# Performance work log

Measured on AMD Instinct MI355X. Metric: run time of the kernel, lower is better.

The kernel has to match this reference:

```python
import jax, jax.numpy as jnp
from jax import lax
import numpy as np

B, DIM, HEADS, H, W = 4, 384, 8, 128, 128


def conv2d(x, w, b, groups=1, pad=0):
    # x: NCHW, w: OIHW (I = in_channels // groups)
    y = lax.conv_general_dilated(
        x, w, window_strides=(1, 1), padding=[(pad, pad), (pad, pad)],
        dimension_numbers=("NCHW", "OIHW", "NCHW"), feature_group_count=groups)
    return y + b[None, :, None, None]


def _l2norm(x, eps=1e-12):
    # torch F.normalize(dim=-1): x / max(||x||_2, eps)
    n = jnp.sqrt(jnp.sum(x * x, axis=-1, keepdims=True))
    return x / jnp.maximum(n, eps)


def setup_inputs() -> dict:
    key = jax.random.key(0)
    ks = jax.random.split(key, 8)
    s = 0.02
    d = DIM
    return {
        "x": jax.random.normal(ks[0], (B, d, H, W), jnp.float32),
        "feature": jax.random.normal(ks[1], (B, d, H, W), jnp.float32),
        "qkv_w": jax.random.normal(ks[2], (3 * d, d, 1, 1), jnp.float32) * s,
        "qkv_b": jnp.zeros((3 * d,), jnp.float32),
        "dw_w": jax.random.normal(ks[3], (3 * d, 1, 3, 3), jnp.float32) * s,  # depthwise, groups=3d
        "dw_b": jnp.zeros((3 * d,), jnp.float32),
        "qdw_w": jax.random.normal(ks[4], (2 * d, 1, 3, 3), jnp.float32) * s,  # depthwise, groups=2d
        "qdw_b": jnp.zeros((2 * d,), jnp.float32),
        "qpw_w": jax.random.normal(ks[5], (d, 2 * d, 1, 1), jnp.float32) * s,
        "qpw_b": jnp.zeros((d,), jnp.float32),
        "proj_w": jax.random.normal(ks[6], (d, d, 1, 1), jnp.float32) * s,
        "proj_b": jnp.zeros((d,), jnp.float32),
        "temperature": jnp.ones((HEADS, 1, 1), jnp.float32),
        "K": 24,  # top-k count == int(C * 0.5) with C = DIM // HEADS = 48
    }


def reference(x, feature, qkv_w, qkv_b, dw_w, dw_b, qdw_w, qdw_b,
              qpw_w, qpw_b, proj_w, proj_b, temperature, K):
    b, c, h, w = x.shape
    # qkv = dwconv3x3(conv1x1(x))
    qkv = conv2d(conv2d(x, qkv_w, qkv_b), dw_w, dw_b, groups=3 * c, pad=1)
    q, k, v = jnp.split(qkv, 3, axis=1)
    # q branch: dwconv3x3 on cat([q, feature]) -> GELU(exact) -> 1x1 conv
    qf = conv2d(jnp.concatenate([q, feature], axis=1), qdw_w, qdw_b, groups=2 * c, pad=1)
    qf = jax.nn.gelu(qf, approximate=False)
    q = conv2d(qf, qpw_w, qpw_b)

    def heads(t):
        return t.reshape(b, HEADS, c // HEADS, h * w)  # b head C (h w)

    q = _l2norm(heads(q))
    k = _l2norm(heads(k))
    v = heads(v)
    # channel attention: [b,head,C,C]
    attn = jnp.einsum("bhcn,bhdn->bhcd", q, k) * temperature
    vals, idx = lax.top_k(attn, K)
    neg = jnp.full_like(attn, -jnp.inf)
    attn = jnp.put_along_axis(neg, idx, vals, axis=-1, inplace=False)
    attn = jax.nn.softmax(attn, axis=-1)
    out = jnp.einsum("bhcd,bhdn->bhcn", attn, v).reshape(b, c, h, w)
    return conv2d(out, proj_w, proj_b)
```

## Files before the change

kernel.cpp:

```cpp
#include <hip/hip_runtime.h>

using u16 = unsigned short;
typedef __attribute__((ext_vector_type(8))) __bf16 bf16x8;
typedef __attribute__((ext_vector_type(4))) float  f32x4;
typedef __attribute__((ext_vector_type(8))) u16    u16x8;
typedef __attribute__((ext_vector_type(4))) u16    u16x4;

#define NB   4
#define DIM  384
#define NPIX 16384

__device__ __forceinline__ u16 f2bf(float f) {
  return __builtin_bit_cast(u16, (__bf16)f);
}
__device__ __forceinline__ float bf2f(u16 u) {
  return (float)__builtin_bit_cast(__bf16, u);
}
__device__ __forceinline__ void gload16(const void* g, void* l) {
  __builtin_amdgcn_global_load_lds(
      (const __attribute__((address_space(1))) void*)g,
      (__attribute__((address_space(3))) void*)l, 16, 0, 0);
}

__global__ void k_cvt2(const float* __restrict__ s, u16* __restrict__ hi,
                       u16* __restrict__ lo, int n) {
  int i = blockIdx.x * 256 + threadIdx.x;
  if (i < n) {
    float v = s[i];
    u16 h = f2bf(v);
    hi[i] = h;
    lo[i] = f2bf(v - bf2f(h));
  }
}

__global__ void k_splitx(const float* __restrict__ x, u16* __restrict__ xhi,
                         u16* __restrict__ xlo) {
  __shared__ float tile[64][33];
  const int tid = threadIdx.x;
  const int n0 = blockIdx.x * 32, c0 = blockIdx.y * 64, b = blockIdx.z;
  const int tj = tid & 31, ti = tid >> 5;
  const float* xp = x + ((size_t)b * DIM + c0) * NPIX + n0;
  #pragma unroll
  for (int i = 0; i < 8; ++i) {
    const int c = i * 8 + ti;
    tile[c][tj] = xp[(size_t)c * NPIX + tj];
  }
  __syncthreads();
  const int px = tid >> 3, sl = tid & 7;
  u16x8 ph, pl;
  #pragma unroll
  for (int e = 0; e < 8; ++e) {
    const float v = tile[sl * 8 + e][px];
    const u16 h = f2bf(v);
    ph[e] = h;
    pl[e] = f2bf(v - bf2f(h));
  }
  const size_t off = ((size_t)b * NPIX + n0 + px) * DIM + c0 + sl * 8;
  *(u16x8*)(xhi + off) = ph;
  *(u16x8*)(xlo + off) = pl;
}

template<int OUTMODE>
__global__ __launch_bounds__(256, 4)
void k_gemmS(const u16* __restrict__ A, const u16* __restrict__ B,
             void* __restrict__ Out, const float* __restrict__ bias,
             int M, int N, int Kd, size_t Astride)
{
  __shared__ u16 lA[128 * 64];
  __shared__ u16 lB[128 * 64];
  const int tid = threadIdx.x, wid = tid >> 6, lane = tid & 63;
  const int GX = gridDim.x, GY = gridDim.y;
  const int W = GX * GY * (int)gridDim.z;
  const int w = blockIdx.x + GX * (blockIdx.y + GY * blockIdx.z);
  const int nw = (w & 7) * (W >> 3) + (w >> 3);
  const int mt = nw % GY;
  const int rest = nw / GY;
  const int ntile = rest % GX;
  const int b = rest / GX;
  const int m0 = mt * 128, n0 = ntile * 128;

  const int srow = lane >> 3;
  const int sslot = (lane & 7) ^ srow;
  const size_t rowA = (size_t)(m0 + wid * 32 + srow) * Kd + sslot * 8 +
                      (size_t)b * Astride;
  const size_t rowB = ((size_t)b * N + n0 + wid * 32 + srow) * Kd + sslot * 8;
  u16* lAw = &lA[(wid * 32) * 64];
  u16* lBw = &lB[(wid * 32) * 64];
  const int wm = (wid & 1) * 64, wn = (wid >> 1) * 64;
  const int cl = lane & 15, rl = lane >> 4;
  const int sxa = cl & 7;

  f32x4 acc[4][4];
  const f32x4 fz = {0.f, 0.f, 0.f, 0.f};
  #pragma unroll
  for (int i = 0; i < 4; ++i)
    #pragma unroll
    for (int j = 0; j < 4; ++j) acc[i][j] = fz;

  const int nk = Kd >> 6;
  for (int kt = 0; kt < nk; ++kt) {
    const u16* Ap = A + rowA + kt * 64;
    const u16* Bp = B + rowB + kt * 64;
    __syncthreads();
    #pragma unroll
    for (int i = 0; i < 4; ++i) {
      gload16(Ap + (size_t)(i * 8) * Kd, lAw + i * 8 * 64);
      gload16(Bp + (size_t)(i * 8) * Kd, lBw + i * 8 * 64);
    }
    __syncthreads();
    #pragma unroll
    for (int ks = 0; ks < 2; ++ks) {
      bf16x8 av[4], bv[4];
      #pragma unroll
      for (int i = 0; i < 4; ++i) {
        av[i] = *(const bf16x8*)&lA[(wm + i * 16 + cl) * 64 + ((ks * 4 + rl) ^ sxa) * 8];
        bv[i] = *(const bf16x8*)&lB[(wn + i * 16 + cl) * 64 + ((ks * 4 + rl) ^ sxa) * 8];
      }
      #pragma unroll
      for (int i = 0; i < 4; ++i)
        #pragma unroll
        for (int j = 0; j < 4; ++j)
          acc[i][j] = __builtin_amdgcn_mfma_f32_16x16x32_bf16(av[i], bv[j], acc[i][j], 0, 0, 0);
    }
  }

  #pragma unroll
  for (int i = 0; i < 4; ++i) {
    #pragma unroll
    for (int j = 0; j < 4; ++j) {
      #pragma unroll
      for (int r = 0; r < 4; ++r) {
        const int m = m0 + wm + i * 16 + rl * 4 + r;
        const int n = n0 + wn + j * 16 + cl;
        const float v = acc[i][j][r] + bias[m];
        const size_t o = ((size_t)b * M + m) * N + n;
        if (OUTMODE == 0) ((float*)Out)[o] = v;
        else ((u16*)Out)[o] = f2bf(v);
      }
    }
  }
}

template<int OUTMODE, bool SSQ>
__global__ __launch_bounds__(256, 4)
void k_gemmP(const u16* __restrict__ Ahi, const u16* __restrict__ Alo,
             const u16* __restrict__ Bhi, const u16* __restrict__ Blo,
             void* __restrict__ Out, u16* __restrict__ OutLo,
             const float* __restrict__ bias, float* __restrict__ ssq,
             int M, int N, int Kd)
{
  __shared__ u16 lA[128 * 64];
  __shared__ u16 lB[128 * 64];
  const int tid = threadIdx.x, wid = tid >> 6, lane = tid & 63;
  const int GX = gridDim.x, GY = gridDim.y;
  const int W = GX * GY * (int)gridDim.z;
  const int w = blockIdx.x + GX * (blockIdx.y + GY * blockIdx.z);
  const int nw = (w & 7) * (W >> 3) + (w >> 3);
  const int mt = nw % GY;
  const int rest = nw / GY;
  const int ntile = rest % GX;
  const int b = rest / GX;
  const int m0 = mt * 128, n0 = ntile * 128;

  const int srow = lane >> 3;
  const int sp = (lane & 7) ^ srow;
  const int scol = (sp & 3) * 8;
  const u16* baseA = (sp < 4) ? Ahi : Alo;
  const u16* baseB = (sp < 4) ? Bhi : Blo;
  const u16* srcA[4];
  const u16* srcB[4];
  #pragma unroll
  for (int i = 0; i < 4; ++i) {
    srcA[i] = baseA + (size_t)(m0 + wid * 32 + i * 8 + srow) * Kd + scol;
    srcB[i] = baseB + ((size_t)b * N + n0 + wid * 32 + i * 8 + srow) * Kd + scol;
  }
  u16* lAw = &lA[(wid * 32) * 64];
  u16* lBw = &lB[(wid * 32) * 64];
  const int wm = (wid & 1) * 64, wn = (wid >> 1) * 64;
  const int cl = lane & 15, rl = lane >> 4;
  const int ph = rl ^ (cl & 7);

  f32x4 acc[4][4];
  const f32x4 fz = {0.f, 0.f, 0.f, 0.f};
  #pragma unroll
  for (int i = 0; i < 4; ++i)
    #pragma unroll
    for (int j = 0; j < 4; ++j) acc[i][j] = fz;

  const int nk = Kd >> 5;
  for (int kt = 0; kt < nk; ++kt) {
    __syncthreads();
    #pragma unroll
    for (int i = 0; i < 4; ++i) {
      gload16(srcA[i] + kt * 32, lAw + i * 8 * 64);
      gload16(srcB[i] + kt * 32, lBw + i * 8 * 64);
    }
    __syncthreads();
    bf16x8 avh[4], bvh[4], avl[4], bvl[4];
    #pragma unroll
    for (int i = 0; i < 4; ++i) {
      avh[i] = *(const bf16x8*)&lA[(wm + i * 16 + cl) * 64 + ph * 8];
      bvh[i] = *(const bf16x8*)&lB[(wn + i * 16 + cl) * 64 + ph * 8];
    }
    #pragma unroll
    for (int i = 0; i < 4; ++i)
      #pragma unroll
      for (int j = 0; j < 4; ++j)
        acc[i][j] = __builtin_amdgcn_mfma_f32_16x16x32_bf16(avh[i], bvh[j], acc[i][j], 0, 0, 0);
    #pragma unroll
    for (int i = 0; i < 4; ++i)
      avl[i] = *(const bf16x8*)&lA[(wm + i * 16 + cl) * 64 + (ph ^ 4) * 8];
    #pragma unroll
    for (int i = 0; i < 4; ++i)
      #pragma unroll
      for (int j = 0; j < 4; ++j)
        acc[i][j] = __builtin_amdgcn_mfma_f32_16x16x32_bf16(avl[i], bvh[j], acc[i][j], 0, 0, 0);
    #pragma unroll
    for (int i = 0; i < 4; ++i)
      bvl[i] = *(const bf16x8*)&lB[(wn + i * 16 + cl) * 64 + (ph ^ 4) * 8];
    #pragma unroll
    for (int i = 0; i < 4; ++i)
      #pragma unroll
      for (int j = 0; j < 4; ++j)
        acc[i][j] = __builtin_amdgcn_mfma_f32_16x16x32_bf16(avh[i], bvl[j], acc[i][j], 0, 0, 0);
  }

  float sq[4][4];
  if (SSQ) {
    #pragma unroll
    for (int i = 0; i < 4; ++i)
      #pragma unroll
      for (int r = 0; r < 4; ++r) sq[i][r] = 0.f;
  }
  #pragma unroll
  for (int i = 0; i < 4; ++i) {
    #pragma unroll
    for (int j = 0; j < 4; ++j) {
      #pragma unroll
      for (int r = 0; r < 4; ++r) {
        const int m = m0 + wm + i * 16 + rl * 4 + r;
        const int n = n0 + wn + j * 16 + cl;
        const float v = acc[i][j][r] + bias[m];
        if (SSQ) sq[i][r] += v * v;
        const size_t o = ((size_t)b * M + m) * N + n;
        if (OUTMODE == 0) ((float*)Out)[o] = v;
        else {
          u16 h = f2bf(v);
          ((u16*)Out)[o] = h;
          OutLo[o] = f2bf(v - bf2f(h));
        }
      }
    }
  }
  if (SSQ) {
    #pragma unroll
    for (int i = 0; i < 4; ++i) {
      #pragma unroll
      for (int r = 0; r < 4; ++r) {
        float s = sq[i][r];
        s += __shfl_xor(s, 1);
        s += __shfl_xor(s, 2);
        s += __shfl_xor(s, 4);
        s += __shfl_xor(s, 8);
        if (cl == 0)
          atomicAdd(&ssq[(size_t)b * M + m0 + wm + i * 16 + rl * 4 + r], s);
      }
    }
  }
}

__device__ __forceinline__ void row_acc_f32(const float* __restrict__ rowp,
    int x0, float w0, float w1, float w2,
    float& o0, float& o1, float& o2, float& o3)
{
  float4 r = *(const float4*)(rowp + x0);
  float lm = __shfl_up(r.w, 1);   if (x0 == 0)   lm = 0.f;
  float rt = __shfl_down(r.x, 1); if (x0 == 124) rt = 0.f;
  o0 = fmaf(lm,  w0, fmaf(r.x, w1, fmaf(r.y, w2, o0)));
  o1 = fmaf(r.x, w0, fmaf(r.y, w1, fmaf(r.z, w2, o1)));
  o2 = fmaf(r.y, w0, fmaf(r.z, w1, fmaf(r.w, w2, o2)));
  o3 = fmaf(r.z, w0, fmaf(r.w, w1, fmaf(rt,  w2, o3)));
}
__device__ __forceinline__ void row_acc_bf16(const u16* __restrict__ rowp,
    int x0, float w0, float w1, float w2,
    float& o0, float& o1, float& o2, float& o3)
{
  u16x4 rv = *(const u16x4*)(rowp + x0);
  float r0 = bf2f(rv[0]), r1 = bf2f(rv[1]), r2 = bf2f(rv[2]), r3 = bf2f(rv[3]);
  float lm = __shfl_up(r3, 1);   if (x0 == 0)   lm = 0.f;
  float rt = __shfl_down(r0, 1); if (x0 == 124) rt = 0.f;
  o0 = fmaf(lm, w0, fmaf(r0, w1, fmaf(r1, w2, o0)));
  o1 = fmaf(r0, w0, fmaf(r1, w1, fmaf(r2, w2, o1)));
  o2 = fmaf(r1, w0, fmaf(r2, w1, fmaf(r3, w2, o2)));
  o3 = fmaf(r2, w0, fmaf(r3, w1, fmaf(rt, w2, o3)));
}

__global__ __launch_bounds__(256, 4)
void k_dw3qk(const float* __restrict__ src, const float* __restrict__ w9,
             const float* __restrict__ bias, float* __restrict__ qdwbuf,
             u16* __restrict__ khi, u16* __restrict__ klo,
             float* __restrict__ ssqk)
{
  const int tid = threadIdx.x, wv = tid >> 6, lane = tid & 63;
  const int whw = blockIdx.x + 16 * (blockIdx.y + 96 * blockIdx.z);
  const int g = (whw & 7) + 8 * (whw >> 7);
  const int xchunk = (whw >> 3) & 15;
  const int cg = g % 96, b = g / 96;
  const int n0 = xchunk * 1024 + tid * 4;
  const int h = n0 >> 7, x0 = n0 & 127;
  const int c0 = cg * 8;
  const int hm = (h > 0) ? h - 1 : 0, hp = (h < 127) ? h + 1 : 127;
  const float topf = (h > 0) ? 1.f : 0.f, botf = (h < 127) ? 1.f : 0.f;
  const float* base = src + ((size_t)b * 768 + c0) * NPIX;
  const bool isk = (c0 >= 384);
  float ssl[8];
  #pragma unroll
  for (int s = 0; s < 8; ++s) {
    const int c = c0 + s;
    const float* sp = base + (size_t)s * NPIX;
    const float* wc = w9 + c * 9;
    const float bz = bias[c];
    float o0 = bz, o1 = bz, o2 = bz, o3 = bz;
    row_acc_f32(sp + hm * 128, x0, wc[0] * topf, wc[1] * topf, wc[2] * topf, o0, o1, o2, o3);
    row_acc_f32(sp + h  * 128, x0, wc[3], wc[4], wc[5], o0, o1, o2, o3);
    row_acc_f32(sp + hp * 128, x0, wc[6] * botf, wc[7] * botf, wc[8] * botf, o0, o1, o2, o3);
    if (!isk) {
      float4 ov = make_float4(o0, o1, o2, o3);
      *(float4*)(qdwbuf + ((size_t)b * 384 + c) * NPIX + n0) = ov;
      ssl[s] = 0.f;
    } else {
      ssl[s] = o0 * o0 + o1 * o1 + o2 * o2 + o3 * o3;
      u16x4 ph, pl;
      float oo[4] = {o0, o1, o2, o3};
      #pragma unroll
      for (int j = 0; j < 4; ++j) {
        u16 hv = f2bf(oo[j]);
        ph[j] = hv;
        pl[j] = f2bf(oo[j] - bf2f(hv));
      }
      const size_t off = ((size_t)b * 384 + (c - 384)) * NPIX + n0;
      *(u16x4*)(khi + off) = ph;
      *(u16x4*)(klo + off) = pl;
    }
  }
  if (isk) {
    __shared__ float sred[4][8];
    #pragma unroll
    for (int s = 0; s < 8; ++s) {
      float v = ssl[s];
      #pragma unroll
      for (int off = 32; off; off >>= 1) v += __shfl_down(v, off);
      if (lane == 0) sred[wv][s] = v;
    }
    __syncthreads();
    if (tid < 8) {
      float t = sred[0][tid] + sred[1][tid] + sred[2][tid] + sred[3][tid];
      atomicAdd(&ssqk[(size_t)b * DIM + (c0 - 384) + tid], t);
    }
  }
}

__global__ __launch_bounds__(512, 4)
void k_dw3vT(const u16* __restrict__ src, const float* __restrict__ w9,
             const float* __restrict__ bias, u16* __restrict__ vT)
{
  __shared__ u16 th[256 * 64];
  const int tid = threadIdx.x, wv = tid >> 6, lane = tid & 63;
  const int whw = blockIdx.x + 64 * (blockIdx.y + 6 * blockIdx.z);
  const int g = (whw & 7) + 8 * (whw >> 9);
  const int xchunk = (whw >> 3) & 63;
  const int cg = g % 6, b = g / 6;
  const int npx0 = xchunk * 256;
  const int n0 = npx0 + lane * 4;
  const int h = n0 >> 7, x0 = n0 & 127;
  const int c0 = cg * 64 + wv * 8;
  const int hm = (h > 0) ? h - 1 : 0, hp = (h < 127) ? h + 1 : 127;
  const float topf = (h > 0) ? 1.f : 0.f, botf = (h < 127) ? 1.f : 0.f;
  const u16* base = src + ((size_t)b * 384 + c0) * NPIX;
  u16x8 vh[4];
  #pragma unroll
  for (int s = 0; s < 8; ++s) {
    const int c = c0 + s;
    const u16* sp = base + (size_t)s * NPIX;
    const float* wc = w9 + c * 9;
    const float bz = bias[c];
    float o0 = bz, o1 = bz, o2 = bz, o3 = bz;
    row_acc_bf16(sp + hm * 128, x0, wc[0] * topf, wc[1] * topf, wc[2] * topf, o0, o1, o2, o3);
    row_acc_bf16(sp + h  * 128, x0, wc[3], wc[4], wc[5], o0, o1, o2, o3);
    row_acc_bf16(sp + hp * 128, x0, wc[6] * botf, wc[7] * botf, wc[8] * botf, o0, o1, o2, o3);
    vh[0][s] = f2bf(o0); vh[1][s] = f2bf(o1);
    vh[2][s] = f2bf(o2); vh[3][s] = f2bf(o3);
  }
  const int sl = (wv ^ (lane & 7)) * 8;
  #pragma unroll
  for (int j = 0; j < 4; ++j) {
    const int px = lane * 4 + j;
    *(u16x8*)&th[px * 64 + sl] = vh[j];
  }
  __syncthreads();
  if (tid < 256) {
    const int px = tid;
    u16* dst = vT + ((size_t)b * NPIX + npx0 + px) * 384 + cg * 64;
    const int rsw = (px >> 2) & 7;
    #pragma unroll
    for (int s = 0; s < 8; ++s)
      *(u16x8*)(dst + s * 8) = *(const u16x8*)&th[px * 64 + ((s ^ rsw) * 8)];
  }
}

__global__ __launch_bounds__(512, 4)
void k_qdw2(const float* __restrict__ qdwbuf, const float* __restrict__ feat,
            const float* __restrict__ w9, const float* __restrict__ bias,
            u16* __restrict__ qfhi, u16* __restrict__ qflo)
{
  __shared__ u16 th[256 * 64];
  __shared__ u16 tl[256 * 64];
  const int tid = threadIdx.x, wv = tid >> 6, lane = tid & 63;
  const int whw = blockIdx.x + 64 * (blockIdx.y + 12 * blockIdx.z);
  const int g = (whw & 7) + 8 * (whw >> 9);
  const int xchunk = (whw >> 3) & 63;
  const int cg = g % 12, b = g / 12;
  const int npx0 = xchunk * 256;
  const int n0 = npx0 + lane * 4;
  const int h = n0 >> 7, x0 = n0 & 127;
  const int c0 = cg * 64 + wv * 8;
  const int hm = (h > 0) ? h - 1 : 0, hp = (h < 127) ? h + 1 : 127;
  const float topf = (h > 0) ? 1.f : 0.f, botf = (h < 127) ? 1.f : 0.f;
  const bool isq = (c0 < 384);
  const float* base = isq ? (qdwbuf + ((size_t)b * 384 + c0) * NPIX)
                          : (feat   + ((size_t)b * 384 + (c0 - 384)) * NPIX);
  u16x8 vh[4], vl[4];
  #pragma unroll
  for (int s = 0; s < 8; ++s) {
    const int c = c0 + s;
    const float* sp = base + (size_t)s * NPIX;
    const float* wc = w9 + c * 9;
    const float bz = bias[c];
    float o0 = bz, o1 = bz, o2 = bz, o3 = bz;
    row_acc_f32(sp + hm * 128, x0, wc[0] * topf, wc[1] * topf, wc[2] * topf, o0, o1, o2, o3);
    row_acc_f32(sp + h  * 128, x0, wc[3], wc[4], wc[5], o0, o1, o2, o3);
    row_acc_f32(sp + hp * 128, x0, wc[6] * botf, wc[7] * botf, wc[8] * botf, o0, o1, o2, o3);
    float oo[4] = {o0, o1, o2, o3};
    #pragma unroll
    for (int j = 0; j < 4; ++j) {
      const float a = oo[j];
      const float g2 = 0.5f * a * (1.0f + erff(a * 0.70710678118654752440f));
      const u16 hv = f2bf(g2);
      vh[j][s] = hv;
      vl[j][s] = f2bf(g2 - bf2f(hv));
    }
  }
  const int sl = (wv ^ (lane & 7)) * 8;
  #pragma unroll
  for (int j = 0; j < 4; ++j) {
    const int px = lane * 4 + j;
    *(u16x8*)&th[px * 64 + sl] = vh[j];
    *(u16x8*)&tl[px * 64 + sl] = vl[j];
  }
  __syncthreads();
  const int sel = tid >> 8;
  const int px = tid & 255;
  const u16* srcb = sel ? tl : th;
  u16* dst = (sel ? qflo : qfhi) +
             ((size_t)b * NPIX + npx0 + px) * 768 + cg * 64;
  const int rsw = (px >> 2) & 7;
  #pragma unroll
  for (int s = 0; s < 8; ++s)
    *(u16x8*)(dst + s * 8) = *(const u16x8*)&srcb[px * 64 + ((s ^ rsw) * 8)];
}

__global__ __launch_bounds__(256)
void k_qk3(const u16* __restrict__ qhi, const u16* __restrict__ qlo,
           const u16* __restrict__ khi, const u16* __restrict__ klo,
           float* __restrict__ part)
{
  const int wid = threadIdx.x >> 6, lane = threadIdx.x & 63;
  const int bh = blockIdx.y;
  const int b = bh >> 3, hd = bh & 7;
  const size_t base = ((size_t)b * 384 + hd * 48) * NPIX;
  const int cl = lane & 15, rl = lane >> 4;
  f32x4 acc[3][3];
  const f32x4 fz = {0.f, 0.f, 0.f, 0.f};
  #pragma unroll
  for (int i = 0; i < 3; ++i)
    #pragma unroll
    for (int j = 0; j < 3; ++j) acc[i][j] = fz;
  for (int ck = 0; ck < 2; ++ck) {
    const int n0 = (blockIdx.x * 2 + ck) * 512 + wid * 128;
    #pragma unroll
    for (int ks = 0; ks < 4; ++ks) {
      const int nn = n0 + ks * 32 + rl * 8;
      bf16x8 ah[3], al[3], bh16[3], bl16[3];
      #pragma unroll
      for (int i = 0; i < 3; ++i) {
        const size_t ro = base + (size_t)(i * 16 + cl) * NPIX + nn;
        ah[i]   = *(const bf16x8*)&qhi[ro];
        al[i]   = *(const bf16x8*)&qlo[ro];
        bh16[i] = *(const bf16x8*)&khi[ro];
        bl16[i] = *(const bf16x8*)&klo[ro];
      }
      #pragma unroll
      for (int i = 0; i < 3; ++i)
        #pragma unroll
        for (int j = 0; j < 3; ++j) {
          acc[i][j] = __builtin_amdgcn_mfma_f32_16x16x32_bf16(ah[i], bh16[j], acc[i][j], 0, 0, 0);
          acc[i][j] = __builtin_amdgcn_mfma_f32_16x16x32_bf16(ah[i], bl16[j], acc[i][j], 0, 0, 0);
          acc[i][j] = __builtin_amdgcn_mfma_f32_16x16x32_bf16(al[i], bh16[j], acc[i][j], 0, 0, 0);
        }
    }
  }
  float* pp = part + ((size_t)bh * 64 + blockIdx.x * 4 + wid) * 2304;
  #pragma unroll
  for (int i = 0; i < 3; ++i)
    #pragma unroll
    for (int j = 0; j < 3; ++j)
      #pragma unroll
      for (int r = 0; r < 4; ++r)
        pp[(i * 16 + rl * 4 + r) * 48 + (j * 16 + cl)] = acc[i][j][r];
}

__global__ void k_qkred(const float* __restrict__ part, float* __restrict__ raw)
{
  const int bh = blockIdx.x;
  const int p = blockIdx.y * 256 + threadIdx.x;
  const float* pp = part + (size_t)bh * 64 * 2304 + p;
  float s = 0.f;
  #pragma unroll 8
  for (int w = 0; w < 64; ++w) s += pp[(size_t)w * 2304];
  raw[(size_t)bh * 2304 + p] = s;
}

__global__ void k_attn2(const float* __restrict__ raw, const float* __restrict__ ssq_q,
                        const float* __restrict__ ssq_k, const float* __restrict__ temp,
                        const int* __restrict__ Kp, const float* __restrict__ W,
                        u16* __restrict__ WaHi)
{
  __shared__ float at[48 * 49];
  const int bh = blockIdx.x, b = bh >> 3, hd = bh & 7;
  const int tid = threadIdx.x, wv = tid >> 6, lane = tid & 63;
  const int K = *Kp;
  const int d = lane;
  const bool act = (d < 48);
  const float ki = act ? 1.0f / fmaxf(sqrtf(ssq_k[b * DIM + hd * 48 + d]), 1e-12f) : 0.f;
  const float tmp = temp[hd];
  for (int r = 0; r < 12; ++r) {
    const int c = wv * 12 + r;
    const float qi = tmp / fmaxf(sqrtf(ssq_q[b * DIM + hd * 48 + c]), 1e-12f);
    const float v = act ? raw[(size_t)bh * 2304 + c * 48 + d] * qi * ki : -3.0e38f;
    int rank = 0;
    #pragma unroll
    for (int e = 0; e < 48; ++e) {
      const float ve = __shfl(v, e);
      rank += (ve > v || (ve == v && e < d)) ? 1 : 0;
    }
    const bool keep = act && (rank < K);
    float mx = keep ? v : -3.0e38f;
    #pragma unroll
    for (int off = 32; off; off >>= 1) mx = fmaxf(mx, __shfl_xor(mx, off));
    const float ex = keep ? expf(v - mx) : 0.f;
    float sum = ex;
    #pragma unroll
    for (int off = 32; off; off >>= 1) sum += __shfl_xor(sum, off);
    const float rs = 1.0f / sum;
    if (act) at[c * 49 + d] = ex * rs;
  }
  __syncthreads();
  for (int idx = tid; idx < 384 * 48; idx += 256) {
    const int m = idx / 48, dd = idx - m * 48;
    const float* wr = W + (size_t)m * 384 + hd * 48;
    float s = 0.f;
    #pragma unroll
    for (int c = 0; c < 48; ++c) s += wr[c] * at[c * 49 + dd];
    WaHi[((size_t)b * 384 + m) * 384 + hd * 48 + dd] = f2bf(s);
  }
}

extern "C" void kernel_launch(void* const* d_in, const int* in_sizes, int n_in,
                              void* d_out, int out_size, void* d_ws, size_t ws_size,
                              hipStream_t stream)
{
  (void)in_sizes; (void)n_in; (void)out_size; (void)ws_size;
  const float* x      = (const float*)d_in[0];
  const float* feat   = (const float*)d_in[1];
  const float* qkv_w  = (const float*)d_in[2];
  const float* qkv_b  = (const float*)d_in[3];
  const float* dw_w   = (const float*)d_in[4];
  const float* dw_b   = (const float*)d_in[5];
  const float* qdw_w  = (const float*)d_in[6];
  const float* qdw_b  = (const float*)d_in[7];
  const float* qpw_w  = (const float*)d_in[8];
  const float* qpw_b  = (const float*)d_in[9];
  const float* proj_w = (const float*)d_in[10];
  const float* proj_b = (const float*)d_in[11];
  const float* temp   = (const float*)d_in[12];
  const int*   Kp     = (const int*)d_in[13];

  char* ws = (char*)d_ws;
  const size_t HALF = 50331648;

  u16* WqkvHi = (u16*)ws;
  u16* WqkvLo = WqkvHi + 1152 * 384;
  u16* WqpwHi = WqkvLo + 1152 * 384;
  u16* WqpwLo = WqpwHi + 384 * 768;
  float* ssqQ = (float*)(ws + 3244032);
  float* ssqK = ssqQ + NB * DIM;
  float* raw  = ssqK + NB * DIM;
  u16* WaHi   = (u16*)(ws + (4ull << 20));
  char* R1 = ws + (16ull << 20);
  u16* xThi = (u16*)R1;
  u16* xTlo = (u16*)(R1 + HALF);
  float* qdwbuf = (float*)R1;
  u16* qHi = (u16*)R1;
  u16* qLo = (u16*)(R1 + HALF);
  char* R2 = ws + (112ull << 20);
  float* qkpre = (float*)R2;
  u16* qfHi = (u16*)R2;
  u16* qfLo = (u16*)(R2 + 2 * HALF);
  float* part = (float*)R2;
  u16* vT   = (u16*)R2;
  u16* vpre = (u16*)(ws + (304ull << 20));
  u16* kHi = (u16*)d_out;
  u16* kLo = kHi + (size_t)NB * DIM * NPIX;

  hipMemsetAsync(ssqQ, 0, 2 * NB * DIM * sizeof(float), stream);
  k_cvt2<<<dim3(1728), 256, 0, stream>>>(qkv_w, WqkvHi, WqkvLo, 1152 * 384);
  k_cvt2<<<dim3(1152), 256, 0, stream>>>(qpw_w, WqpwHi, WqpwLo, 384 * 768);
  k_splitx<<<dim3(512, 6, NB), 256, 0, stream>>>(x, xThi, xTlo);
  k_gemmP<0, false><<<dim3(128, 6, NB), 256, 0, stream>>>(WqkvHi, WqkvLo, xThi, xTlo,
      (void*)qkpre, nullptr, qkv_b, nullptr, 768, NPIX, 384);
  k_gemmS<1><<<dim3(128, 3, NB), 256, 0, stream>>>(WqkvHi + (size_t)768 * 384,
      xThi, (void*)vpre, qkv_b + 768, 384, NPIX, 384, 0);
  k_dw3qk<<<dim3(16, 96, NB), 256, 0, stream>>>(qkpre, dw_w, dw_b, qdwbuf, kHi, kLo, ssqK);
  k_qdw2<<<dim3(64, 12, NB), 512, 0, stream>>>(qdwbuf, feat, qdw_w, qdw_b, qfHi, qfLo);
  k_gemmP<2, true><<<dim3(128, 3, NB), 256, 0, stream>>>(WqpwHi, WqpwLo, qfHi, qfLo,
      (void*)qHi, qLo, qpw_b, ssqQ, 384, NPIX, 768);
  k_qk3<<<dim3(16, 32), 256, 0, stream>>>(qHi, qLo, kHi, kLo, part);
  k_qkred<<<dim3(32, 9), 256, 0, stream>>>(part, raw);
  k_attn2<<<dim3(32), 256, 0, stream>>>(raw, ssqQ, ssqK, temp, Kp, proj_w, WaHi);
  k_dw3vT<<<dim3(64, 6, NB), 512, 0, stream>>>(vpre, dw_w + 768 * 9, dw_b + 768, vT);
  k_gemmS<0><<<dim3(128, 3, NB), 256, 0, stream>>>(WaHi, vT,
      d_out, proj_b, 384, NPIX, 384, (size_t)384 * 384);
}
```

Baseline: 813.4 us.

## Double-buffer LDS in split-bf16 GEMM with async prefetch two tiles ahead

Turns the k_gemmP main loop into a two-stage LDS pipeline. Global-to-LDS loads for tile kt+2 are issued right after tile kt's MFMAs, and explicit vmcnt waits plus raw barriers replace the paired __syncthreads, so memory latency overlaps compute. The doubled LDS footprint lowers the launch-bounds occupancy hint from 4 to 2 blocks per CU, which reduces latency hiding across blocks. The vmcnt(8) count relies on each thread issuing exactly 8 loads per stage.

```diff
diff --git a/kernel.cpp b/kernel.cpp
--- a/kernel.cpp
+++ b/kernel.cpp
@@ -142,15 +142,15 @@
 }
 
 template<int OUTMODE, bool SSQ>
-__global__ __launch_bounds__(256, 4)
+__global__ __launch_bounds__(256, 2)
 void k_gemmP(const u16* __restrict__ Ahi, const u16* __restrict__ Alo,
              const u16* __restrict__ Bhi, const u16* __restrict__ Blo,
              void* __restrict__ Out, u16* __restrict__ OutLo,
              const float* __restrict__ bias, float* __restrict__ ssq,
              int M, int N, int Kd)
 {
-  __shared__ u16 lA[128 * 64];
-  __shared__ u16 lB[128 * 64];
+  __shared__ u16 lA[2][128 * 64];
+  __shared__ u16 lB[2][128 * 64];
   const int tid = threadIdx.x, wid = tid >> 6, lane = tid & 63;
   const int GX = gridDim.x, GY = gridDim.y;
   const int W = GX * GY * (int)gridDim.z;
@@ -174,8 +174,7 @@
     srcA[i] = baseA + (size_t)(m0 + wid * 32 + i * 8 + srow) * Kd + scol;
     srcB[i] = baseB + ((size_t)b * N + n0 + wid * 32 + i * 8 + srow) * Kd + scol;
   }
-  u16* lAw = &lA[(wid * 32) * 64];
-  u16* lBw = &lB[(wid * 32) * 64];
+  const int woff = (wid * 32) * 64;
   const int wm = (wid & 1) * 64, wn = (wid >> 1) * 64;
   const int cl = lane & 15, rl = lane >> 4;
   const int ph = rl ^ (cl & 7);
@@ -188,19 +187,33 @@
     for (int j = 0; j < 4; ++j) acc[i][j] = fz;
 
   const int nk = Kd >> 5;
+
+  #pragma unroll
+  for (int i = 0; i < 4; ++i) {
+    gload16(srcA[i], &lA[0][woff + i * 8 * 64]);
+    gload16(srcB[i], &lB[0][woff + i * 8 * 64]);
+  }
+  #pragma unroll
+  for (int i = 0; i < 4; ++i) {
+    gload16(srcA[i] + 32, &lA[1][woff + i * 8 * 64]);
+    gload16(srcB[i] + 32, &lB[1][woff + i * 8 * 64]);
+  }
+
   for (int kt = 0; kt < nk; ++kt) {
-    __syncthreads();
+    if (kt + 1 < nk) {
+      asm volatile("s_waitcnt vmcnt(8)" ::: "memory");
+    } else {
+      asm volatile("s_waitcnt vmcnt(0)" ::: "memory");
+    }
+    __builtin_amdgcn_s_barrier();
+    __builtin_amdgcn_sched_barrier(0);
+    const u16* bA = lA[kt & 1];
+    const u16* bB = lB[kt & 1];
+    bf16x8 avh[4], bvh[4], avl[4], bvl[4];
     #pragma unroll
     for (int i = 0; i < 4; ++i) {
-      gload16(srcA[i] + kt * 32, lAw + i * 8 * 64);
-      gload16(srcB[i] + kt * 32, lBw + i * 8 * 64);
-    }
-    __syncthreads();
-    bf16x8 avh[4], bvh[4], avl[4], bvl[4];
-    #pragma unroll
-    for (int i = 0; i < 4; ++i) {
-      avh[i] = *(const bf16x8*)&lA[(wm + i * 16 + cl) * 64 + ph * 8];
-      bvh[i] = *(const bf16x8*)&lB[(wn + i * 16 + cl) * 64 + ph * 8];
+      avh[i] = *(const bf16x8*)&bA[(wm + i * 16 + cl) * 64 + ph * 8];
+      bvh[i] = *(const bf16x8*)&bB[(wn + i * 16 + cl) * 64 + ph * 8];
     }
     #pragma unroll
     for (int i = 0; i < 4; ++i)
@@ -209,7 +222,7 @@
         acc[i][j] = __builtin_amdgcn_mfma_f32_16x16x32_bf16(avh[i], bvh[j], acc[i][j], 0, 0, 0);
     #pragma unroll
     for (int i = 0; i < 4; ++i)
-      avl[i] = *(const bf16x8*)&lA[(wm + i * 16 + cl) * 64 + (ph ^ 4) * 8];
+      avl[i] = *(const bf16x8*)&bA[(wm + i * 16 + cl) * 64 + (ph ^ 4) * 8];
     #pragma unroll
     for (int i = 0; i < 4; ++i)
       #pragma unroll
@@ -217,12 +230,22 @@
         acc[i][j] = __builtin_amdgcn_mfma_f32_16x16x32_bf16(avl[i], bvh[j], acc[i][j], 0, 0, 0);
     #pragma unroll
     for (int i = 0; i < 4; ++i)
-      bvl[i] = *(const bf16x8*)&lB[(wn + i * 16 + cl) * 64 + (ph ^ 4) * 8];
+      bvl[i] = *(const bf16x8*)&bB[(wn + i * 16 + cl) * 64 + (ph ^ 4) * 8];
     #pragma unroll
     for (int i = 0; i < 4; ++i)
       #pragma unroll
       for (int j = 0; j < 4; ++j)
         acc[i][j] = __builtin_amdgcn_mfma_f32_16x16x32_bf16(avh[i], bvl[j], acc[i][j], 0, 0, 0);
+    __builtin_amdgcn_s_barrier();
+    __builtin_amdgcn_sched_barrier(0);
+    if (kt + 2 < nk) {
+      const int kb = kt & 1;
+      #pragma unroll
+      for (int i = 0; i < 4; ++i) {
+        gload16(srcA[i] + (kt + 2) * 32, &lA[kb][woff + i * 8 * 64]);
+        gload16(srcB[i] + (kt + 2) * 32, &lB[kb][woff + i * 8 * 64]);
+      }
+    }
   }
 
   float sq[4][4];
```

Result: slower. 847.8 us (+4.2%).
